# Kernel tuning notes

Hardware: AMD Instinct MI355X
Metric: run time of the kernel (lower is better)

## Reference

```python
import jax, jax.numpy as jnp
import numpy as np

N = 50000
E = 800000
IN_C, HID_C, OUT_C = 512, 128, 256


def setup_inputs() -> dict:
    key = jax.random.key(0)
    k1, k2, k3, k4, k5, k6 = jax.random.split(key, 6)
    x = jax.random.normal(k1, (N, IN_C), dtype=jnp.float32)
    edge_index = jax.random.randint(k2, (2, E), 0, N, dtype=jnp.int64)
    # Linear weights stored torch-style as [out, in]; bias per layer
    w1 = jax.random.normal(k3, (HID_C, IN_C), dtype=jnp.float32) * (1.0 / np.sqrt(IN_C))
    b1 = jax.random.normal(k4, (HID_C,), dtype=jnp.float32) * 0.02
    w2 = jax.random.normal(k5, (OUT_C, HID_C), dtype=jnp.float32) * (1.0 / np.sqrt(HID_C))
    b2 = jax.random.normal(k6, (OUT_C,), dtype=jnp.float32) * 0.02
    return {"x": x, "edge_index": edge_index, "w1": w1, "b1": b1, "w2": w2, "b2": b2}


def gcn_conv(x, edge_index, w, b):
    # x: [N, Cin], w: [Cout, Cin] (torch Linear layout), b: [Cout]
    h = x @ w.T                              # [N, Cout]
    src, dst = edge_index[0], edge_index[1]
    msgs = h[src]                            # gather: [E, Cout]
    agg = jax.ops.segment_sum(msgs, dst, num_segments=h.shape[0])  # scatter_add
    return agg + b


def reference(x, edge_index, w1, b1, w2, b2):
    h = gcn_conv(x, edge_index, w1, b1)
    h = jax.nn.relu(h)
    out = gcn_conv(h, edge_index, w2, b2)
    return out
```

## Files before the change

### kernel.cpp

```cpp
#include <hip/hip_runtime.h>

#define NN 50000
#define EE 800000
#define INC 512
#define HIDC 128
#define OUTC 256
#define CAP 64
#define OV_CAP 65536
#define BUILD_BLOCKS 196
#define GB1 782

typedef __attribute__((ext_vector_type(8))) short bf16x8;
typedef __attribute__((ext_vector_type(4))) float f32x4;

__device__ __forceinline__ short f2bf(float f) {
    unsigned u = __float_as_uint(f);
    unsigned r = u + 0x7fff + ((u >> 16) & 1);
    return (short)(r >> 16);
}
__device__ __forceinline__ float bf2f(short s) {
    return __uint_as_float(((unsigned)(unsigned short)s) << 16);
}

template<bool IN_BF16, bool ADDBIAS, bool OUT_BF16>
__device__ __forceinline__ void gemm_core(
    const void* __restrict__ Av, const float* __restrict__ B,
    const float* __restrict__ bias, void* __restrict__ Cv,
    int M, int Nc, int K, int bx, int by,
    short As[64][72], short Bs[128][72])
{
    int tid = threadIdx.x;
    int lane = tid & 63, wave = tid >> 6;
    int row0 = bx * 64, col0 = by * 128;
    int wm = (wave & 1) * 32, wn = (wave >> 1) * 64;
    int l16 = lane & 15, quad = lane >> 4;

    f32x4 acc[2][4];
#pragma unroll
    for (int i = 0; i < 2; i++)
#pragma unroll
        for (int j = 0; j < 4; j++) acc[i][j] = {0.f, 0.f, 0.f, 0.f};

    for (int k0 = 0; k0 < K; k0 += 64) {
        if (IN_BF16) {
            const short* A = (const short*)Av;
#pragma unroll
            for (int w = 0; w < 2; w++) {
                int f = tid + w * 256;
                int rr = f >> 3, c8 = f & 7;
                int gr = row0 + rr;
                bf16x8 v = {0, 0, 0, 0, 0, 0, 0, 0};
                if (gr < M) v = *(const bf16x8*)&A[(long)gr * K + k0 + c8 * 8];
                *(bf16x8*)&As[rr][c8 * 8] = v;
            }
        } else {
            const float* A = (const float*)Av;
#pragma unroll
            for (int w = 0; w < 4; w++) {
                int f = tid + w * 256;
                int rr = f >> 4, c4 = f & 15;
                int gr = row0 + rr;
                float4 v = make_float4(0.f, 0.f, 0.f, 0.f);
                if (gr < M) v = *(const float4*)&A[(long)gr * K + k0 + c4 * 4];
                short4 s;
                s.x = f2bf(v.x); s.y = f2bf(v.y); s.z = f2bf(v.z); s.w = f2bf(v.w);
                *(short4*)&As[rr][c4 * 4] = s;
            }
        }
#pragma unroll
        for (int w = 0; w < 8; w++) {
            int f = tid + w * 256;
            int rr = f >> 4, c4 = f & 15;
            float4 v = *(const float4*)&B[(long)(col0 + rr) * K + k0 + c4 * 4];
            short4 s;
            s.x = f2bf(v.x); s.y = f2bf(v.y); s.z = f2bf(v.z); s.w = f2bf(v.w);
            *(short4*)&Bs[rr][c4 * 4] = s;
        }
        __syncthreads();

#pragma unroll
        for (int kk = 0; kk < 64; kk += 32) {
            bf16x8 af[2], bfr[4];
#pragma unroll
            for (int i = 0; i < 2; i++)
                af[i] = *(const bf16x8*)&As[wm + i * 16 + l16][kk + quad * 8];
#pragma unroll
            for (int j = 0; j < 4; j++)
                bfr[j] = *(const bf16x8*)&Bs[wn + j * 16 + l16][kk + quad * 8];
#pragma unroll
            for (int i = 0; i < 2; i++)
#pragma unroll
                for (int j = 0; j < 4; j++)
                    acc[i][j] = __builtin_amdgcn_mfma_f32_16x16x32_bf16(
                        af[i], bfr[j], acc[i][j], 0, 0, 0);
        }
        __syncthreads();
    }

#pragma unroll
    for (int i = 0; i < 2; i++) {
#pragma unroll
        for (int rr = 0; rr < 4; rr++) {
            int grow = row0 + wm + i * 16 + quad * 4 + rr;
            if (grow < M) {
#pragma unroll
                for (int j = 0; j < 4; j++) {
                    int gcol = col0 + wn + j * 16 + l16;
                    float v = acc[i][j][rr];
                    if (ADDBIAS) v += bias[gcol];
                    if (OUT_BF16)
                        ((short*)Cv)[(long)grow * Nc + gcol] = f2bf(v);
                    else
                        ((float*)Cv)[(long)grow * Nc + gcol] = v;
                }
            }
        }
    }
}

__global__ __launch_bounds__(256) void fat_build_gemm1(
    const int* __restrict__ ei, int* __restrict__ cnt,
    unsigned short* __restrict__ bucket, int* __restrict__ ovcnt,
    int* __restrict__ ovlist,
    const float* __restrict__ x, const float* __restrict__ w1,
    short* __restrict__ h)
{
    __shared__ short As[64][72];
    __shared__ short Bs[128][72];

    if (blockIdx.x < BUILD_BLOCKS) {
        int t = threadIdx.x;
        long base = ((long)blockIdx.x * 256 + t) * 16;
        if (base + 16 <= EE) {
            int4 sv[4], dv[4];
#pragma unroll
            for (int q = 0; q < 4; q++) {
                sv[q] = *(const int4*)&ei[base + q * 4];
                dv[q] = *(const int4*)&ei[EE + base + q * 4];
            }
            const int* sp = (const int*)sv;
            const int* dp = (const int*)dv;
#pragma unroll
            for (int k = 0; k < 16; k++) {
                int src = sp[k], dst = dp[k];
                int pos = atomicAdd(&cnt[dst], 1);
                if (pos < CAP) bucket[(long)dst * CAP + pos] = (unsigned short)src;
                else {
                    int o = atomicAdd(ovcnt, 1);
                    if (o < OV_CAP) { ovlist[o * 2] = src; ovlist[o * 2 + 1] = dst; }
                }
            }
        } else {
            for (int k = 0; k < 16; k++) {
                long e = base + k;
                if (e < EE) {
                    int src = ei[e], dst = ei[EE + e];
                    int pos = atomicAdd(&cnt[dst], 1);
                    if (pos < CAP) bucket[(long)dst * CAP + pos] = (unsigned short)src;
                    else {
                        int o = atomicAdd(ovcnt, 1);
                        if (o < OV_CAP) { ovlist[o * 2] = src; ovlist[o * 2 + 1] = dst; }
                    }
                }
            }
        }
    } else {
        gemm_core<false, false, true>(x, w1, nullptr, h, NN, HIDC, INC,
                                      blockIdx.x - BUILD_BLOCKS, 0, As, Bs);
    }
}

__global__ __launch_bounds__(256) void gemm2_k(
    const short* __restrict__ r2, const float* __restrict__ w2,
    const float* __restrict__ b2, float* __restrict__ out)
{
    __shared__ short As[64][72];
    __shared__ short Bs[128][72];
    gemm_core<true, true, false>(r2, w2, b2, out, NN, OUTC, HIDC,
                                 blockIdx.x, blockIdx.y, As, Bs);
}

template<bool RELU>
__global__ __launch_bounds__(256) void gather_k(
    const short* __restrict__ hsrc, const unsigned short* __restrict__ bucket,
    const int* __restrict__ cnt, const float* __restrict__ bias,
    float* __restrict__ aggf, short* __restrict__ rout)
{
    int t = threadIdx.x;
    int node = blockIdx.x * 16 + (t >> 4);
    int c8 = t & 15;
    if (node >= NN) return;
    int m = cnt[node]; if (m > CAP) m = CAP;
    const unsigned short* bk = bucket + (long)node * CAP;
    float acc[8];
#pragma unroll
    for (int k = 0; k < 8; k++) acc[k] = 0.f;
    int j = 0;
    for (; j + 4 <= m; j += 4) {
        int s0 = bk[j], s1 = bk[j + 1], s2 = bk[j + 2], s3 = bk[j + 3];
        bf16x8 v0 = *(const bf16x8*)&hsrc[((long)s0 << 7) + c8 * 8];
        bf16x8 v1 = *(const bf16x8*)&hsrc[((long)s1 << 7) + c8 * 8];
        bf16x8 v2 = *(const bf16x8*)&hsrc[((long)s2 << 7) + c8 * 8];
        bf16x8 v3 = *(const bf16x8*)&hsrc[((long)s3 << 7) + c8 * 8];
#pragma unroll
        for (int k = 0; k < 8; k++)
            acc[k] += bf2f(v0[k]) + bf2f(v1[k]) + bf2f(v2[k]) + bf2f(v3[k]);
    }
    for (; j < m; j++) {
        int s0 = bk[j];
        bf16x8 v0 = *(const bf16x8*)&hsrc[((long)s0 << 7) + c8 * 8];
#pragma unroll
        for (int k = 0; k < 8; k++) acc[k] += bf2f(v0[k]);
    }
    if (RELU) {
        *(float4*)&aggf[((long)node << 7) + c8 * 8] =
            make_float4(acc[0], acc[1], acc[2], acc[3]);
        *(float4*)&aggf[((long)node << 7) + c8 * 8 + 4] =
            make_float4(acc[4], acc[5], acc[6], acc[7]);
        bf16x8 o;
#pragma unroll
        for (int k = 0; k < 8; k++)
            o[k] = f2bf(fmaxf(acc[k] + bias[c8 * 8 + k], 0.f));
        *(bf16x8*)&rout[((long)node << 7) + c8 * 8] = o;
    } else {
        bf16x8 o;
#pragma unroll
        for (int k = 0; k < 8; k++) o[k] = f2bf(acc[k]);
        *(bf16x8*)&rout[((long)node << 7) + c8 * 8] = o;
    }
}

__global__ __launch_bounds__(128) void ovfix1_k(
    const short* __restrict__ h, const float* __restrict__ b1,
    const int* __restrict__ ovcnt, const int* __restrict__ ovlist,
    float* __restrict__ agg1, short* __restrict__ r)
{
    int n = *ovcnt; if (n > OV_CAP) n = OV_CAP;
    int c = threadIdx.x;
    for (int i = 0; i < n; i++) {
        int src = ovlist[i * 2], dst = ovlist[i * 2 + 1];
        agg1[(long)dst * 128 + c] += bf2f(h[(long)src * 128 + c]);
    }
    __syncthreads();
    for (int i = 0; i < n; i++) {
        int dst = ovlist[i * 2 + 1];
        r[(long)dst * 128 + c] =
            f2bf(fmaxf(agg1[(long)dst * 128 + c] + b1[c], 0.f));
    }
}

__global__ __launch_bounds__(128) void ovfix2_k(
    const short* __restrict__ r, const unsigned short* __restrict__ bucket,
    const int* __restrict__ cnt, const int* __restrict__ ovcnt,
    const int* __restrict__ ovlist, short* __restrict__ r2)
{
    int n = *ovcnt; if (n > OV_CAP) n = OV_CAP;
    int c = threadIdx.x;
    for (int i = 0; i < n; i++) {
        int dst = ovlist[i * 2 + 1];
        bool dup = false;
        for (int i2 = 0; i2 < i; i2++)
            if (ovlist[i2 * 2 + 1] == dst) { dup = true; break; }
        if (dup) continue;
        int m = cnt[dst]; if (m > CAP) m = CAP;
        const unsigned short* bk = bucket + (long)dst * CAP;
        float acc = 0.f;
        for (int j = 0; j < m; j++)
            acc += bf2f(r[(long)bk[j] * 128 + c]);
        for (int i2 = 0; i2 < n; i2++)
            if (ovlist[i2 * 2 + 1] == dst)
                acc += bf2f(r[(long)ovlist[i2 * 2] * 128 + c]);
        r2[(long)dst * 128 + c] = f2bf(acc);
    }
}

extern "C" void kernel_launch(void* const* d_in, const int* in_sizes, int n_in,
                              void* d_out, int out_size, void* d_ws, size_t ws_size,
                              hipStream_t stream) {
    const float* x  = (const float*)d_in[0];
    const int*   ei = (const int*)d_in[1];
    const float* w1 = (const float*)d_in[2];
    const float* b1 = (const float*)d_in[3];
    const float* w2 = (const float*)d_in[4];
    const float* b2 = (const float*)d_in[5];
    float* out = (float*)d_out;

    char* ws = (char*)d_ws;
    size_t off = 0;
    short* h    = (short*)(ws + off); off += (size_t)NN * HIDC * 2;
    float* agg1 = (float*)(ws + off); off += (size_t)NN * HIDC * 4;
    short* r    = (short*)(ws + off); off += (size_t)NN * HIDC * 2;
    short* r2   = (short*)(ws + off); off += (size_t)NN * HIDC * 2;
    unsigned short* bucket = (unsigned short*)(ws + off);
    off += (size_t)NN * CAP * 2;
    int* cnt    = (int*)(ws + off);   off += (size_t)NN * 4;
    int* ovcnt  = (int*)(ws + off);   off += 256;
    int* ovlist = (int*)(ws + off);   off += (size_t)OV_CAP * 2 * 4;

    hipMemsetAsync(cnt, 0, (size_t)NN * 4 + 4, stream);

    dim3 blk(256);

    fat_build_gemm1<<<dim3(BUILD_BLOCKS + GB1), blk, 0, stream>>>(
        ei, cnt, bucket, ovcnt, ovlist, x, w1, h);

    gather_k<true><<<dim3(3125), blk, 0, stream>>>(h, bucket, cnt, b1, agg1, r);
    ovfix1_k<<<dim3(1), dim3(128), 0, stream>>>(h, b1, ovcnt, ovlist, agg1, r);

    gather_k<false><<<dim3(3125), blk, 0, stream>>>(r, bucket, cnt, nullptr, nullptr, r2);
    ovfix2_k<<<dim3(1), dim3(128), 0, stream>>>(r, bucket, cnt, ovcnt, ovlist, r2);

    gemm2_k<<<dim3(GB1, 2), blk, 0, stream>>>(r2, w2, b2, out);
}
```

Measured before the change: 306.0 us.

## Fuse layer-2 gather into GEMM2, pre-convert weights, spread edge build across GEMM blocks

```diff
diff --git a/kernel.cpp b/kernel.cpp
--- a/kernel.cpp
+++ b/kernel.cpp
@@ -7,7 +7,6 @@
 #define OUTC 256
 #define CAP 64
 #define OV_CAP 65536
-#define BUILD_BLOCKS 196
 #define GB1 782
 
 typedef __attribute__((ext_vector_type(8))) short bf16x8;
@@ -22,139 +21,42 @@
     return __uint_as_float(((unsigned)(unsigned short)s) << 16);
 }
 
-template<bool IN_BF16, bool ADDBIAS, bool OUT_BF16>
-__device__ __forceinline__ void gemm_core(
-    const void* __restrict__ Av, const float* __restrict__ B,
-    const float* __restrict__ bias, void* __restrict__ Cv,
-    int M, int Nc, int K, int bx, int by,
-    short As[64][72], short Bs[128][72])
-{
-    int tid = threadIdx.x;
-    int lane = tid & 63, wave = tid >> 6;
-    int row0 = bx * 64, col0 = by * 128;
-    int wm = (wave & 1) * 32, wn = (wave >> 1) * 64;
-    int l16 = lane & 15, quad = lane >> 4;
-
-    f32x4 acc[2][4];
-#pragma unroll
-    for (int i = 0; i < 2; i++)
-#pragma unroll
-        for (int j = 0; j < 4; j++) acc[i][j] = {0.f, 0.f, 0.f, 0.f};
-
-    for (int k0 = 0; k0 < K; k0 += 64) {
-        if (IN_BF16) {
-            const short* A = (const short*)Av;
-#pragma unroll
-            for (int w = 0; w < 2; w++) {
-                int f = tid + w * 256;
-                int rr = f >> 3, c8 = f & 7;
-                int gr = row0 + rr;
-                bf16x8 v = {0, 0, 0, 0, 0, 0, 0, 0};
-                if (gr < M) v = *(const bf16x8*)&A[(long)gr * K + k0 + c8 * 8];
-                *(bf16x8*)&As[rr][c8 * 8] = v;
-            }
-        } else {
-            const float* A = (const float*)Av;
-#pragma unroll
-            for (int w = 0; w < 4; w++) {
-                int f = tid + w * 256;
-                int rr = f >> 4, c4 = f & 15;
-                int gr = row0 + rr;
-                float4 v = make_float4(0.f, 0.f, 0.f, 0.f);
-                if (gr < M) v = *(const float4*)&A[(long)gr * K + k0 + c4 * 4];
-                short4 s;
-                s.x = f2bf(v.x); s.y = f2bf(v.y); s.z = f2bf(v.z); s.w = f2bf(v.w);
-                *(short4*)&As[rr][c4 * 4] = s;
-            }
-        }
-#pragma unroll
-        for (int w = 0; w < 8; w++) {
-            int f = tid + w * 256;
-            int rr = f >> 4, c4 = f & 15;
-            float4 v = *(const float4*)&B[(long)(col0 + rr) * K + k0 + c4 * 4];
-            short4 s;
-            s.x = f2bf(v.x); s.y = f2bf(v.y); s.z = f2bf(v.z); s.w = f2bf(v.w);
-            *(short4*)&Bs[rr][c4 * 4] = s;
-        }
-        __syncthreads();
-
-#pragma unroll
-        for (int kk = 0; kk < 64; kk += 32) {
-            bf16x8 af[2], bfr[4];
-#pragma unroll
-            for (int i = 0; i < 2; i++)
-                af[i] = *(const bf16x8*)&As[wm + i * 16 + l16][kk + quad * 8];
-#pragma unroll
-            for (int j = 0; j < 4; j++)
-                bfr[j] = *(const bf16x8*)&Bs[wn + j * 16 + l16][kk + quad * 8];
-#pragma unroll
-            for (int i = 0; i < 2; i++)
-#pragma unroll
-                for (int j = 0; j < 4; j++)
-                    acc[i][j] = __builtin_amdgcn_mfma_f32_16x16x32_bf16(
-                        af[i], bfr[j], acc[i][j], 0, 0, 0);
-        }
-        __syncthreads();
-    }
-
-#pragma unroll
-    for (int i = 0; i < 2; i++) {
-#pragma unroll
-        for (int rr = 0; rr < 4; rr++) {
-            int grow = row0 + wm + i * 16 + quad * 4 + rr;
-            if (grow < M) {
-#pragma unroll
-                for (int j = 0; j < 4; j++) {
-                    int gcol = col0 + wn + j * 16 + l16;
-                    float v = acc[i][j][rr];
-                    if (ADDBIAS) v += bias[gcol];
-                    if (OUT_BF16)
-                        ((short*)Cv)[(long)grow * Nc + gcol] = f2bf(v);
-                    else
-                        ((float*)Cv)[(long)grow * Nc + gcol] = v;
-                }
-            }
-        }
-    }
+__global__ __launch_bounds__(256) void cvt_w(
+    const float* __restrict__ w1, const float* __restrict__ w2,
+    short* __restrict__ w1b, short* __restrict__ w2b)
+{
+    int gid = blockIdx.x * 256 + threadIdx.x;
+    float4 v;
+    short4* dst;
+    if (gid < 16384) { v = ((const float4*)w1)[gid]; dst = &((short4*)w1b)[gid]; }
+    else             { v = ((const float4*)w2)[gid - 16384]; dst = &((short4*)w2b)[gid - 16384]; }
+    short4 s;
+    s.x = f2bf(v.x); s.y = f2bf(v.y); s.z = f2bf(v.z); s.w = f2bf(v.w);
+    *dst = s;
 }
 
 __global__ __launch_bounds__(256) void fat_build_gemm1(
     const int* __restrict__ ei, int* __restrict__ cnt,
     unsigned short* __restrict__ bucket, int* __restrict__ ovcnt,
     int* __restrict__ ovlist,
-    const float* __restrict__ x, const float* __restrict__ w1,
+    const float* __restrict__ x, const short* __restrict__ w1b,
     short* __restrict__ h)
 {
     __shared__ short As[64][72];
     __shared__ short Bs[128][72];
 
-    if (blockIdx.x < BUILD_BLOCKS) {
-        int t = threadIdx.x;
-        long base = ((long)blockIdx.x * 256 + t) * 16;
-        if (base + 16 <= EE) {
-            int4 sv[4], dv[4];
-#pragma unroll
-            for (int q = 0; q < 4; q++) {
-                sv[q] = *(const int4*)&ei[base + q * 4];
-                dv[q] = *(const int4*)&ei[EE + base + q * 4];
-            }
-            const int* sp = (const int*)sv;
-            const int* dp = (const int*)dv;
-#pragma unroll
-            for (int k = 0; k < 16; k++) {
-                int src = sp[k], dst = dp[k];
-                int pos = atomicAdd(&cnt[dst], 1);
-                if (pos < CAP) bucket[(long)dst * CAP + pos] = (unsigned short)src;
-                else {
-                    int o = atomicAdd(ovcnt, 1);
-                    if (o < OV_CAP) { ovlist[o * 2] = src; ovlist[o * 2 + 1] = dst; }
-                }
-            }
-        } else {
-            for (int k = 0; k < 16; k++) {
-                long e = base + k;
-                if (e < EE) {
-                    int src = ei[e], dst = ei[EE + e];
+    {
+        long base = ((long)blockIdx.x * 256 + threadIdx.x) * 4;
+        if (base < EE) {
+            int4 sv = *(const int4*)&ei[base];
+            int4 dv = *(const int4*)&ei[EE + base];
+            int sp[4] = {sv.x, sv.y, sv.z, sv.w};
+            int dp[4] = {dv.x, dv.y, dv.z, dv.w};
+            int nk = (EE - base >= 4) ? 4 : (int)(EE - base);
+#pragma unroll
+            for (int k = 0; k < 4; k++) {
+                if (k < nk) {
+                    int src = sp[k], dst = dp[k];
                     int pos = atomicAdd(&cnt[dst], 1);
                     if (pos < CAP) bucket[(long)dst * CAP + pos] = (unsigned short)src;
                     else {
@@ -164,27 +66,76 @@
                 }
             }
         }
-    } else {
-        gemm_core<false, false, true>(x, w1, nullptr, h, NN, HIDC, INC,
-                                      blockIdx.x - BUILD_BLOCKS, 0, As, Bs);
-    }
-}
-
-__global__ __launch_bounds__(256) void gemm2_k(
-    const short* __restrict__ r2, const float* __restrict__ w2,
-    const float* __restrict__ b2, float* __restrict__ out)
-{
-    __shared__ short As[64][72];
-    __shared__ short Bs[128][72];
-    gemm_core<true, true, false>(r2, w2, b2, out, NN, OUTC, HIDC,
-                                 blockIdx.x, blockIdx.y, As, Bs);
-}
-
-template<bool RELU>
-__global__ __launch_bounds__(256) void gather_k(
-    const short* __restrict__ hsrc, const unsigned short* __restrict__ bucket,
-    const int* __restrict__ cnt, const float* __restrict__ bias,
-    float* __restrict__ aggf, short* __restrict__ rout)
+    }
+
+    int tid = threadIdx.x;
+    int lane = tid & 63, wave = tid >> 6;
+    int row0 = blockIdx.x * 64;
+    int wm = (wave & 1) * 32, wn = (wave >> 1) * 64;
+    int l16 = lane & 15, quad = lane >> 4;
+
+    f32x4 acc[2][4];
+#pragma unroll
+    for (int i = 0; i < 2; i++)
+#pragma unroll
+        for (int j = 0; j < 4; j++) acc[i][j] = {0.f, 0.f, 0.f, 0.f};
+
+    for (int k0 = 0; k0 < INC; k0 += 64) {
+#pragma unroll
+        for (int w = 0; w < 4; w++) {
+            int f = tid + w * 256;
+            int rr = f >> 4, c4 = f & 15;
+            int gr = row0 + rr;
+            float4 v = make_float4(0.f, 0.f, 0.f, 0.f);
+            if (gr < NN) v = *(const float4*)&x[(long)gr * INC + k0 + c4 * 4];
+            short4 s;
+            s.x = f2bf(v.x); s.y = f2bf(v.y); s.z = f2bf(v.z); s.w = f2bf(v.w);
+            *(short4*)&As[rr][c4 * 4] = s;
+        }
+#pragma unroll
+        for (int w = 0; w < 4; w++) {
+            int f = tid + w * 256;
+            int rr = f >> 3, c8 = f & 7;
+            *(bf16x8*)&Bs[rr][c8 * 8] =
+                *(const bf16x8*)&w1b[(long)rr * INC + k0 + c8 * 8];
+        }
+        __syncthreads();
+
+#pragma unroll
+        for (int kk = 0; kk < 64; kk += 32) {
+            bf16x8 af[2], bfr[4];
+#pragma unroll
+            for (int i = 0; i < 2; i++)
+                af[i] = *(const bf16x8*)&As[wm + i * 16 + l16][kk + quad * 8];
+#pragma unroll
+            for (int j = 0; j < 4; j++)
+                bfr[j] = *(const bf16x8*)&Bs[wn + j * 16 + l16][kk + quad * 8];
+#pragma unroll
+            for (int i = 0; i < 2; i++)
+#pragma unroll
+                for (int j = 0; j < 4; j++)
+                    acc[i][j] = __builtin_amdgcn_mfma_f32_16x16x32_bf16(
+                        af[i], bfr[j], acc[i][j], 0, 0, 0);
+        }
+        __syncthreads();
+    }
+
+#pragma unroll
+    for (int i = 0; i < 2; i++)
+#pragma unroll
+        for (int rr = 0; rr < 4; rr++) {
+            int grow = row0 + wm + i * 16 + quad * 4 + rr;
+            if (grow < NN)
+#pragma unroll
+                for (int j = 0; j < 4; j++)
+                    h[(long)grow * HIDC + wn + j * 16 + l16] = f2bf(acc[i][j][rr]);
+        }
+}
+
+__global__ __launch_bounds__(256) void gather1_k(
+    const short* __restrict__ h, const unsigned short* __restrict__ bucket,
+    const int* __restrict__ cnt, const float* __restrict__ b1,
+    short* __restrict__ r)
 {
     int t = threadIdx.x;
     int node = blockIdx.x * 16 + (t >> 4);
@@ -197,62 +148,146 @@
     for (int k = 0; k < 8; k++) acc[k] = 0.f;
     int j = 0;
     for (; j + 4 <= m; j += 4) {
-        int s0 = bk[j], s1 = bk[j + 1], s2 = bk[j + 2], s3 = bk[j + 3];
-        bf16x8 v0 = *(const bf16x8*)&hsrc[((long)s0 << 7) + c8 * 8];
-        bf16x8 v1 = *(const bf16x8*)&hsrc[((long)s1 << 7) + c8 * 8];
-        bf16x8 v2 = *(const bf16x8*)&hsrc[((long)s2 << 7) + c8 * 8];
-        bf16x8 v3 = *(const bf16x8*)&hsrc[((long)s3 << 7) + c8 * 8];
+        ushort4 ss = *(const ushort4*)&bk[j];
+        bf16x8 v0 = *(const bf16x8*)&h[((long)ss.x << 7) + c8 * 8];
+        bf16x8 v1 = *(const bf16x8*)&h[((long)ss.y << 7) + c8 * 8];
+        bf16x8 v2 = *(const bf16x8*)&h[((long)ss.z << 7) + c8 * 8];
+        bf16x8 v3 = *(const bf16x8*)&h[((long)ss.w << 7) + c8 * 8];
 #pragma unroll
         for (int k = 0; k < 8; k++)
             acc[k] += bf2f(v0[k]) + bf2f(v1[k]) + bf2f(v2[k]) + bf2f(v3[k]);
     }
     for (; j < m; j++) {
-        int s0 = bk[j];
-        bf16x8 v0 = *(const bf16x8*)&hsrc[((long)s0 << 7) + c8 * 8];
+        bf16x8 v0 = *(const bf16x8*)&h[((long)bk[j] << 7) + c8 * 8];
 #pragma unroll
         for (int k = 0; k < 8; k++) acc[k] += bf2f(v0[k]);
     }
-    if (RELU) {
-        *(float4*)&aggf[((long)node << 7) + c8 * 8] =
-            make_float4(acc[0], acc[1], acc[2], acc[3]);
-        *(float4*)&aggf[((long)node << 7) + c8 * 8 + 4] =
-            make_float4(acc[4], acc[5], acc[6], acc[7]);
-        bf16x8 o;
-#pragma unroll
-        for (int k = 0; k < 8; k++)
-            o[k] = f2bf(fmaxf(acc[k] + bias[c8 * 8 + k], 0.f));
-        *(bf16x8*)&rout[((long)node << 7) + c8 * 8] = o;
-    } else {
-        bf16x8 o;
-#pragma unroll
-        for (int k = 0; k < 8; k++) o[k] = f2bf(acc[k]);
-        *(bf16x8*)&rout[((long)node << 7) + c8 * 8] = o;
-    }
+    bf16x8 o;
+#pragma unroll
+    for (int k = 0; k < 8; k++)
+        o[k] = f2bf(fmaxf(acc[k] + b1[c8 * 8 + k], 0.f));
+    *(bf16x8*)&r[((long)node << 7) + c8 * 8] = o;
+}
+
+__global__ __launch_bounds__(256) void gg2_k(
+    const short* __restrict__ r, const unsigned short* __restrict__ bucket,
+    const int* __restrict__ cnt, const short* __restrict__ w2b,
+    const float* __restrict__ b2, float* __restrict__ out)
+{
+    __shared__ short As[64][136];
+    __shared__ short Bs[256][72];
+
+    int tid = threadIdx.x;
+    int node0 = blockIdx.x * 64;
+
+    {
+        int node = node0 + (tid >> 2);
+        int ln = tid & 3;
+        float acc[32];
+#pragma unroll
+        for (int k = 0; k < 32; k++) acc[k] = 0.f;
+        if (node < NN) {
+            int m = cnt[node]; if (m > CAP) m = CAP;
+            const unsigned short* bk = bucket + (long)node * CAP;
+            int j = 0;
+            for (; j + 2 <= m; j += 2) {
+                int s0 = bk[j], s1 = bk[j + 1];
+                const short* p0 = &r[((long)s0 << 7) + ln * 32];
+                const short* p1 = &r[((long)s1 << 7) + ln * 32];
+                bf16x8 a0 = *(const bf16x8*)(p0);
+                bf16x8 a1 = *(const bf16x8*)(p0 + 8);
+                bf16x8 a2 = *(const bf16x8*)(p0 + 16);
+                bf16x8 a3 = *(const bf16x8*)(p0 + 24);
+                bf16x8 c0 = *(const bf16x8*)(p1);
+                bf16x8 c1 = *(const bf16x8*)(p1 + 8);
+                bf16x8 c2 = *(const bf16x8*)(p1 + 16);
+                bf16x8 c3 = *(const bf16x8*)(p1 + 24);
+#pragma unroll
+                for (int k = 0; k < 8; k++) {
+                    acc[k]      += bf2f(a0[k]) + bf2f(c0[k]);
+                    acc[k + 8]  += bf2f(a1[k]) + bf2f(c1[k]);
+                    acc[k + 16] += bf2f(a2[k]) + bf2f(c2[k]);
+                    acc[k + 24] += bf2f(a3[k]) + bf2f(c3[k]);
+                }
+            }
+            for (; j < m; j++) {
+                const short* p0 = &r[((long)bk[j] << 7) + ln * 32];
+#pragma unroll
+                for (int q = 0; q < 4; q++) {
+                    bf16x8 v = *(const bf16x8*)(p0 + q * 8);
+#pragma unroll
+                    for (int k = 0; k < 8; k++) acc[q * 8 + k] += bf2f(v[k]);
+                }
+            }
+        }
+        int nl = tid >> 2;
+#pragma unroll
+        for (int q = 0; q < 4; q++) {
+            bf16x8 s;
+#pragma unroll
+            for (int k = 0; k < 8; k++) s[k] = f2bf(acc[q * 8 + k]);
+            *(bf16x8*)&As[nl][ln * 32 + q * 8] = s;
+        }
+    }
+    __syncthreads();
+
+    int lane = tid & 63, wave = tid >> 6;
+    int wn = wave * 64;
+    int l16 = lane & 15, quad = lane >> 4;
+
+    f32x4 acc[4][4];
+#pragma unroll
+    for (int i = 0; i < 4; i++)
+#pragma unroll
+        for (int j = 0; j < 4; j++) acc[i][j] = {0.f, 0.f, 0.f, 0.f};
+
+    for (int k0 = 0; k0 < HIDC; k0 += 64) {
+#pragma unroll
+        for (int w = 0; w < 8; w++) {
+            int f = tid + w * 256;
+            int rr = f >> 3, c8 = f & 7;
+            *(bf16x8*)&Bs[rr][c8 * 8] =
+                *(const bf16x8*)&w2b[(long)rr * HIDC + k0 + c8 * 8];
+        }
+        __syncthreads();
+#pragma unroll
+        for (int kk = 0; kk < 64; kk += 32) {
+            bf16x8 af[4], bfr[4];
+#pragma unroll
+            for (int i = 0; i < 4; i++)
+                af[i] = *(const bf16x8*)&As[i * 16 + l16][k0 + kk + quad * 8];
+#pragma unroll
+            for (int j = 0; j < 4; j++)
+                bfr[j] = *(const bf16x8*)&Bs[wn + j * 16 + l16][kk + quad * 8];
+#pragma unroll
+            for (int i = 0; i < 4; i++)
+#pragma unroll
+                for (int j = 0; j < 4; j++)
+                    acc[i][j] = __builtin_amdgcn_mfma_f32_16x16x32_bf16(
+                        af[i], bfr[j], acc[i][j], 0, 0, 0);
+        }
+        __syncthreads();
+    }
+
+#pragma unroll
+    for (int i = 0; i < 4; i++)
+#pragma unroll
+        for (int rr = 0; rr < 4; rr++) {
+            int grow = node0 + i * 16 + quad * 4 + rr;
+            if (grow < NN)
+#pragma unroll
+                for (int j = 0; j < 4; j++) {
+                    int gcol = wn + j * 16 + l16;
+                    out[(long)grow * OUTC + gcol] = acc[i][j][rr] + b2[gcol];
+                }
+        }
 }
 
 __global__ __launch_bounds__(128) void ovfix1_k(
     const short* __restrict__ h, const float* __restrict__ b1,
+    const unsigned short* __restrict__ bucket, const int* __restrict__ cnt,
     const int* __restrict__ ovcnt, const int* __restrict__ ovlist,
-    float* __restrict__ agg1, short* __restrict__ r)
-{
-    int n = *ovcnt; if (n > OV_CAP) n = OV_CAP;
-    int c = threadIdx.x;
-    for (int i = 0; i < n; i++) {
-        int src = ovlist[i * 2], dst = ovlist[i * 2 + 1];
-        agg1[(long)dst * 128 + c] += bf2f(h[(long)src * 128 + c]);
-    }
-    __syncthreads();
-    for (int i = 0; i < n; i++) {
-        int dst = ovlist[i * 2 + 1];
-        r[(long)dst * 128 + c] =
-            f2bf(fmaxf(agg1[(long)dst * 128 + c] + b1[c], 0.f));
-    }
-}
-
-__global__ __launch_bounds__(128) void ovfix2_k(
-    const short* __restrict__ r, const unsigned short* __restrict__ bucket,
-    const int* __restrict__ cnt, const int* __restrict__ ovcnt,
-    const int* __restrict__ ovlist, short* __restrict__ r2)
+    short* __restrict__ r)
 {
     int n = *ovcnt; if (n > OV_CAP) n = OV_CAP;
     int c = threadIdx.x;
@@ -266,11 +301,46 @@
         const unsigned short* bk = bucket + (long)dst * CAP;
         float acc = 0.f;
         for (int j = 0; j < m; j++)
-            acc += bf2f(r[(long)bk[j] * 128 + c]);
+            acc += bf2f(h[(long)bk[j] * HIDC + c]);
         for (int i2 = 0; i2 < n; i2++)
             if (ovlist[i2 * 2 + 1] == dst)
-                acc += bf2f(r[(long)ovlist[i2 * 2] * 128 + c]);
-        r2[(long)dst * 128 + c] = f2bf(acc);
+                acc += bf2f(h[(long)ovlist[i2 * 2] * HIDC + c]);
+        r[(long)dst * HIDC + c] = f2bf(fmaxf(acc + b1[c], 0.f));
+    }
+}
+
+__global__ __launch_bounds__(256) void ovfix2_k(
+    const short* __restrict__ r, const unsigned short* __restrict__ bucket,
+    const int* __restrict__ cnt, const int* __restrict__ ovcnt,
+    const int* __restrict__ ovlist, const short* __restrict__ w2b,
+    const float* __restrict__ b2, float* __restrict__ out)
+{
+    __shared__ float row[HIDC];
+    int n = *ovcnt; if (n > OV_CAP) n = OV_CAP;
+    int t = threadIdx.x;
+    for (int i = 0; i < n; i++) {
+        int dst = ovlist[i * 2 + 1];
+        bool dup = false;
+        for (int i2 = 0; i2 < i; i2++)
+            if (ovlist[i2 * 2 + 1] == dst) { dup = true; break; }
+        if (dup) continue;
+        if (t < HIDC) {
+            int m = cnt[dst]; if (m > CAP) m = CAP;
+            const unsigned short* bk = bucket + (long)dst * CAP;
+            float acc = 0.f;
+            for (int j = 0; j < m; j++)
+                acc += bf2f(r[(long)bk[j] * HIDC + t]);
+            for (int i2 = 0; i2 < n; i2++)
+                if (ovlist[i2 * 2 + 1] == dst)
+                    acc += bf2f(r[(long)ovlist[i2 * 2] * HIDC + t]);
+            row[t] = bf2f(f2bf(acc));
+        }
+        __syncthreads();
+        float o = 0.f;
+        for (int c = 0; c < HIDC; c++)
+            o = fmaf(row[c], bf2f(w2b[(long)t * HIDC + c]), o);
+        out[(long)dst * OUTC + t] = o + b2[t];
+        __syncthreads();
     }
 }
 
@@ -288,9 +358,9 @@
     char* ws = (char*)d_ws;
     size_t off = 0;
     short* h    = (short*)(ws + off); off += (size_t)NN * HIDC * 2;
-    float* agg1 = (float*)(ws + off); off += (size_t)NN * HIDC * 4;
     short* r    = (short*)(ws + off); off += (size_t)NN * HIDC * 2;
-    short* r2   = (short*)(ws + off); off += (size_t)NN * HIDC * 2;
+    short* w1b  = (short*)(ws + off); off += (size_t)HIDC * INC * 2;
+    short* w2b  = (short*)(ws + off); off += (size_t)OUTC * HIDC * 2;
     unsigned short* bucket = (unsigned short*)(ws + off);
     off += (size_t)NN * CAP * 2;
     int* cnt    = (int*)(ws + off);   off += (size_t)NN * 4;
@@ -301,14 +371,14 @@
 
     dim3 blk(256);
 
-    fat_build_gemm1<<<dim3(BUILD_BLOCKS + GB1), blk, 0, stream>>>(
-        ei, cnt, bucket, ovcnt, ovlist, x, w1, h);
-
-    gather_k<true><<<dim3(3125), blk, 0, stream>>>(h, bucket, cnt, b1, agg1, r);
-    ovfix1_k<<<dim3(1), dim3(128), 0, stream>>>(h, b1, ovcnt, ovlist, agg1, r);
-
-    gather_k<false><<<dim3(3125), blk, 0, stream>>>(r, bucket, cnt, nullptr, nullptr, r2);
-    ovfix2_k<<<dim3(1), dim3(128), 0, stream>>>(r, bucket, cnt, ovcnt, ovlist, r2);
-
-    gemm2_k<<<dim3(GB1, 2), blk, 0, stream>>>(r2, w2, b2, out);
-}
+    cvt_w<<<dim3(96), blk, 0, stream>>>(w1, w2, w1b, w2b);
+
+    fat_build_gemm1<<<dim3(GB1), blk, 0, stream>>>(
+        ei, cnt, bucket, ovcnt, ovlist, x, w1b, h);
+
+    gather1_k<<<dim3((NN + 15) / 16), blk, 0, stream>>>(h, bucket, cnt, b1, r);
+    ovfix1_k<<<dim3(1), dim3(128), 0, stream>>>(h, b1, bucket, cnt, ovcnt, ovlist, r);
+
+    gg2_k<<<dim3(GB1), blk, 0, stream>>>(r, bucket, cnt, w2b, b2, out);
+    ovfix2_k<<<dim3(1), blk, 0, stream>>>(r, bucket, cnt, ovcnt, ovlist, w2b, b2, out);
+}
```

Result: slower. 324.2 us (+5.9%).
